# Kernel tuning notes

Measured on AMD Instinct MI355X. Metric: run time of the kernel, lower is better.

Reference implementation:

```python
import math
import jax, jax.numpy as jnp
import numpy as np
from jax import lax

MUL_IN, MUL_OUT = 8, 16
DIM_IN, DIM_OUT = 4 * MUL_IN, 4 * MUL_OUT  # 0e(1) + 1o(3) per multiplicity
DIAMETER = 3.0
STEPS = (1.0, 1.0, 1.0)
NUM_RB = 4
BATCH, GRID = 8, 32


def _lattice():
    r = DIAMETER / 2
    axes = [np.arange(-math.floor(r / s), math.floor(r / s) + 1.0) * s for s in STEPS]
    return jnp.asarray(np.stack(np.meshgrid(*axes, indexing='ij'), axis=-1), jnp.float32)  # [X,Y,Z,3]


def _sus(x):
    # smooth unit step: exp(-1/x) for x>0 else 0
    return jnp.where(x > 0.0, jnp.exp(-1.0 / jnp.where(x > 0.0, x, 1.0)), 0.0)


def _radial_emb(lattice):
    # soft_one_hot_linspace, basis='smooth_finite', cutoff=True
    dist = jnp.linalg.norm(lattice, axis=-1)
    values = jnp.linspace(0.0, DIAMETER / 2, NUM_RB + 2)
    step = values[1] - values[0]
    diff = (dist[..., None] - values[1:-1]) / step
    return 1.14136 * jnp.exp(2.0) * _sus(diff + 1.0) * _sus(1.0 - diff)  # [X,Y,Z,NUM_RB]


def _sph(lattice):
    # real spherical harmonics l=0,1; normalize=True, 'component' normalization
    norm = jnp.linalg.norm(lattice, axis=-1, keepdims=True)
    unit = lattice / jnp.where(norm == 0.0, 1.0, norm)
    sh0 = jnp.ones(lattice.shape[:-1] + (1,), lattice.dtype)
    sh1 = jnp.sqrt(jnp.float32(3.0)) * unit
    return sh0, sh1


def setup_inputs() -> dict:
    key = jax.random.key(0)
    ks = jax.random.split(key, 7)
    x = jax.random.normal(ks[0], (BATCH, GRID, GRID, GRID, DIM_IN), jnp.float32)
    w_lin0 = jax.random.normal(ks[1], (MUL_IN, MUL_OUT), jnp.float32)
    w_lin1 = jax.random.normal(ks[2], (MUL_IN, MUL_OUT), jnp.float32)
    pshape = (NUM_RB, MUL_IN, 1, MUL_OUT)
    w000 = jax.random.normal(ks[3], pshape, jnp.float32)
    w011 = jax.random.normal(ks[4], pshape, jnp.float32)
    w101 = jax.random.normal(ks[5], pshape, jnp.float32)
    w110 = jax.random.normal(ks[6], pshape, jnp.float32)
    return dict(x=x, w_lin0=w_lin0, w_lin1=w_lin1, w000=w000, w011=w011, w101=w101, w110=w110)


def _forward(x, w_lin0, w_lin1, w000, w011, w101, w110):
    lattice = _lattice()
    emb = _radial_emb(lattice)
    sh0, sh1 = _sph(lattice)
    n_lat = lattice.shape[0] * lattice.shape[1] * lattice.shape[2]

    # ---- self-connection: FunctionalLinear(irreps_in -> irreps_out), per-l blocks ----
    lin_norm = 1.0 / math.sqrt(MUL_IN)
    x0 = x[..., :MUL_IN]                                             # [B,X,Y,Z,8]
    x1 = x[..., MUL_IN:].reshape(x.shape[:-1] + (MUL_IN, 3))         # [B,X,Y,Z,8,3]
    sc0 = jnp.einsum('...u,uw->...w', x0, w_lin0) * lin_norm
    sc1 = (jnp.einsum('...ui,uw->...wi', x1, w_lin1) * lin_norm).reshape(x.shape[:-1] + (3 * MUL_OUT,))
    sc = jnp.concatenate([sc0, sc1], axis=-1)                        # [B,X,Y,Z,DIM_OUT]

    # ---- radial weights per lattice point: einsum('xyzk,k...->xyz...') / n_lat ----
    def rad(w):
        return jnp.einsum('xyzk,kuvw->xyzuw', emb, w) / n_lat        # sh mul v == 1 squeezed
    r000, r011, r101, r110 = rad(w000), rad(w011), rad(w101), rad(w110)

    # ---- CG tensor-product 'right': build kernel [X,Y,Z, DIM_IN, DIM_OUT] ----
    inv_s3 = 1.0 / math.sqrt(3.0)  # w3j(0,1,1)=w3j(1,0,1)=w3j(1,1,0)=eye/sqrt(3); w3j(0,0,0)=1
    alpha = 1.0 / math.sqrt(2.0 * MUL_IN)  # 2 paths feed each output irrep, fan mul_in each

    eye3 = jnp.eye(3, dtype=x.dtype)
    # in 0e x sh 0e -> out 0e
    k00 = alpha * r000 * sh0[..., 0][..., None, None]                 # [X,Y,Z,8,16]
    # in 0e x sh 1o -> out 1o
    k01 = (alpha * inv_s3) * jnp.einsum('xyzuw,xyzm->xyzuwm', r011, sh1)
    k01 = k01.reshape(k01.shape[:3] + (MUL_IN, 3 * MUL_OUT))          # [X,Y,Z,8,48]
    # in 1o x sh 1o -> out 0e
    k10 = (alpha * inv_s3) * jnp.einsum('xyzuw,xyzi->xyzuiw', r110, sh1)
    k10 = k10.reshape(k10.shape[:3] + (3 * MUL_IN, MUL_OUT))          # [X,Y,Z,24,16]
    # in 1o x sh 0e -> out 1o
    k11 = (alpha * inv_s3) * jnp.einsum('xyzuw,im->xyzuiwm', r101 * sh0[..., 0][..., None, None], eye3)
    k11 = k11.reshape(k11.shape[:3] + (3 * MUL_IN, 3 * MUL_OUT))      # [X,Y,Z,24,48]

    k = jnp.concatenate([
        jnp.concatenate([k00, k01], axis=-1),
        jnp.concatenate([k10, k11], axis=-1),
    ], axis=-2)                                                       # [X,Y,Z,DIM_IN,DIM_OUT]

    conv = lax.conv_general_dilated(
        lhs=x, rhs=k, window_strides=(1, 1, 1), padding='SAME',
        dimension_numbers=('NXYZC', 'XYZIO', 'NXYZC'))
    return sc + conv


def reference(x, w_lin0, w_lin1, w000, w011, w101, w110):
    return _forward(x, w_lin0, w_lin1, w000, w011, w101, w110)
```

## Files before the change

### kernel.cpp

```cpp
#include <hip/hip_runtime.h>


typedef __attribute__((ext_vector_type(8))) short bf16x8;
typedef __attribute__((ext_vector_type(4))) float f32x4;
typedef unsigned int u32;

__device__ __forceinline__ float sus_f(float v) { return v > 0.f ? __expf(-1.f / v) : 0.f; }

__device__ __forceinline__ unsigned short f2bf(float f) {
    union { float f; unsigned u; } c; c.f = f;
    unsigned u = c.u;
    u += 0x7FFFu + ((u >> 16) & 1u);
    return (unsigned short)(u >> 16);
}

__global__ __launch_bounds__(256) void prep_k(
    const float* __restrict__ w_lin0, const float* __restrict__ w_lin1,
    const float* __restrict__ w000,  const float* __restrict__ w011,
    const float* __restrict__ w101,  const float* __restrict__ w110,
    unsigned short* __restrict__ kw)
{
    const int taps[19] = {1,3,4,5,7,9,10,11,12,13,14,15,16,17,19,21,22,23,25};
    const int ta = blockIdx.x;
    const int t = taps[ta];
    const int a = t / 9, b = (t / 3) % 3, c = t % 3;

    const float fx = (float)(a - 1), fy = (float)(b - 1), fz = (float)(c - 1);
    const float dist = sqrtf(fx * fx + fy * fy + fz * fz);
    float emb[4];
    #pragma unroll
    for (int r = 0; r < 4; ++r) {
        const float v = 0.3f * (float)(r + 1);
        const float d = (dist - v) * (1.0f / 0.3f);
        emb[r] = 8.4335731f * sus_f(d + 1.f) * sus_f(1.f - d);
    }
    const float s = (dist > 0.f) ? (1.7320508f / dist) : 0.f;
    const float shv[3] = { fx * s, fy * s, fz * s };
    const float S000 = 0.25f / 27.f;
    const float S1   = 0.25f * 0.57735027f / 27.f;
    const float LNRM = 0.35355339f;

    const int tid = threadIdx.x;
    const int ci = tid >> 3;

    #pragma unroll
    for (int j = 0; j < 8; ++j) {
        const int o = (tid & 7) * 8 + j;
        float val;
        if (ci < 8) {
            const int u = ci;
            if (o < 16) {
                const float* p = w000 + u * 16 + o;
                val = S000 * (emb[0]*p[0] + emb[1]*p[128] + emb[2]*p[256] + emb[3]*p[384]);
                if (t == 13) val += LNRM * w_lin0[u * 16 + o];
            } else {
                const int oo = o - 16, w = oo / 3, m = oo % 3;
                const float* p = w011 + u * 16 + w;
                val = S1 * shv[m] * (emb[0]*p[0] + emb[1]*p[128] + emb[2]*p[256] + emb[3]*p[384]);
            }
        } else {
            const int iu = ci - 8, u = iu / 3, ic = iu % 3;
            if (o < 16) {
                const float* p = w110 + u * 16 + o;
                val = S1 * shv[ic] * (emb[0]*p[0] + emb[1]*p[128] + emb[2]*p[256] + emb[3]*p[384]);
            } else {
                const int oo = o - 16, w = oo / 3, m = oo % 3;
                if (ic == m) {
                    const float* p = w101 + u * 16 + w;
                    val = S1 * (emb[0]*p[0] + emb[1]*p[128] + emb[2]*p[256] + emb[3]*p[384]);
                    if (t == 13) val += LNRM * w_lin1[u * 16 + w];
                } else {
                    val = 0.f;
                }
            }
        }
        const int g = ci >> 3, slot = ci & 7, nt = o >> 4, cc = o & 15;
        const int lane = (g << 4) | cc;
        kw[((size_t)(ta * 4 + nt) * 64 + lane) * 8 + slot] = f2bf(val);
    }
}

__global__ __launch_bounds__(256) void xcvt(
    const float* __restrict__ x, unsigned short* __restrict__ xb)
{
    const int gi = blockIdx.x * 256 + threadIdx.x;
    const int vox = gi >> 2, g = gi & 3;
    const int gz = vox & 31;
    const float4* sp = reinterpret_cast<const float4*>(x) + (size_t)gi * 2;
    const float4 lo = sp[0], hi = sp[1];
    bf16x8 w;
    w[0] = (short)f2bf(lo.x); w[1] = (short)f2bf(lo.y);
    w[2] = (short)f2bf(lo.z); w[3] = (short)f2bf(lo.w);
    w[4] = (short)f2bf(hi.x); w[5] = (short)f2bf(hi.y);
    w[6] = (short)f2bf(hi.z); w[7] = (short)f2bf(hi.w);
    const int slot = g ^ (((gz + 1) >> 1) & 3);
    const size_t dst = ((size_t)(vox >> 5) << 10) + (gz << 5) + (slot << 3);
    *reinterpret_cast<bf16x8*>(xb + dst) = w;
}

template<bool DIRECT>
__global__ __launch_bounds__(256, 2) void conv_mfma(
    const float* __restrict__ x,
    const unsigned short* __restrict__ xb,
    const unsigned short* __restrict__ kw,
    float* __restrict__ out)
{
    __shared__ unsigned short lx[3 * 10 * 34 * 32];

    const int tid = threadIdx.x;
    const int bid = blockIdx.x;
    const int xcd = bid & 7, idx = bid >> 3;
    const int gid = xcd * 128 + idx;
    const int n = gid >> 7, X = (gid >> 2) & 31, Yg = gid & 3;
    const int Y0 = Yg * 8;
    const int wid = tid >> 6, l = tid & 63, lr = l & 15, lg = l >> 4;

    f32x4* lz = reinterpret_cast<f32x4*>(lx);
    #pragma unroll
    for (int i = 0; i < 16; ++i) {
        const int j = tid + i * 256;
        if (j < 4080) lz[j] = (f32x4)0.f;
    }
    __syncthreads();

    if (DIRECT) {
        #pragma unroll
        for (int k = 0; k < 8; ++k) {
            const int rr = wid + (k << 2);
            if (rr < 30) {
                const int dx = rr / 10, y6 = rr - dx * 10;
                const int gx = X + dx - 1, gy = Y0 + y6 - 1;
                if ((unsigned)gx < 32u && (unsigned)gy < 32u) {
                    const char* src = reinterpret_cast<const char*>(xb) +
                        ((size_t)((n * 32 + gx) * 32 + gy) << 11);
                    char* dstrow = reinterpret_cast<char*>(lx) + rr * 2176 + 64;
                    __builtin_amdgcn_global_load_lds(
                        (const __attribute__((address_space(1))) u32*)(src + l * 16),
                        (__attribute__((address_space(3))) u32*)(dstrow), 16, 0, 0);
                    __builtin_amdgcn_global_load_lds(
                        (const __attribute__((address_space(1))) u32*)(src + 1024 + l * 16),
                        (__attribute__((address_space(3))) u32*)(dstrow + 1024), 16, 0, 0);
                }
            }
        }
    } else {
        for (int it = tid; it < 960; it += 256) {
            const int dx = it / 320, rem = it - dx * 320;
            const int y6 = rem >> 5, z = rem & 31;
            const int gx = X + dx - 1, gy = Y0 + y6 - 1;
            if ((unsigned)gx < 32u && (unsigned)gy < 32u) {
                const float4* sp = reinterpret_cast<const float4*>(
                    x + ((size_t)(((n * 32 + gx) * 32 + gy) * 32 + z) << 5));
                const int swz = ((z + 1) >> 1) & 3;
                char* row = reinterpret_cast<char*>(lx) + (dx * 10 + y6) * 2176 + (z + 1) * 64;
                #pragma unroll
                for (int g = 0; g < 4; ++g) {
                    const float4 lo = sp[2 * g], hi = sp[2 * g + 1];
                    bf16x8 w;
                    w[0] = (short)f2bf(lo.x); w[1] = (short)f2bf(lo.y);
                    w[2] = (short)f2bf(lo.z); w[3] = (short)f2bf(lo.w);
                    w[4] = (short)f2bf(hi.x); w[5] = (short)f2bf(hi.y);
                    w[6] = (short)f2bf(hi.z); w[7] = (short)f2bf(hi.w);
                    *reinterpret_cast<bf16x8*>(row + ((g ^ swz) << 4)) = w;
                }
            }
        }
    }
    __syncthreads();

    constexpr int TA[19] = {1,3,4,5,7,9,10,11,12,13,14,15,16,17,19,21,22,23,25};
    const bf16x8* kwf = reinterpret_cast<const bf16x8*>(kw);
    const char* lxc = reinterpret_cast<const char*>(lx);
    const int yloc = wid * 2;

    f32x4 acc[4][4];
    #pragma unroll
    for (int r = 0; r < 4; ++r)
        #pragma unroll
        for (int nt = 0; nt < 4; ++nt) acc[r][nt] = (f32x4)0.f;

    bf16x8 bcur[4];
    #pragma unroll
    for (int nt = 0; nt < 4; ++nt) bcur[nt] = kwf[(size_t)nt * 64 + l];

    #pragma unroll
    for (int ta = 0; ta < 19; ++ta) {
        const int t = TA[ta];
        const int a = t / 9, b = (t / 3) % 3, c = t % 3;

        bf16x8 bnext[4];
        if (ta < 18) {
            #pragma unroll
            for (int nt = 0; nt < 4; ++nt)
                bnext[nt] = kwf[(size_t)((ta + 1) * 4 + nt) * 64 + l];
        }

        #pragma unroll
        for (int r = 0; r < 4; ++r) {
            const int y10 = yloc + (r >> 1) + b;
            const int zp = 16 * (r & 1) + lr + c;
            const int byte = ((a * 10 + y10) * 34 + zp) * 64 + ((lg ^ ((zp >> 1) & 3)) << 4);
            const bf16x8 af = *reinterpret_cast<const bf16x8*>(lxc + byte);
            #pragma unroll
            for (int nt = 0; nt < 4; ++nt)
                acc[r][nt] = __builtin_amdgcn_mfma_f32_16x16x32_bf16(af, bcur[nt], acc[r][nt], 0, 0, 0);
        }

        if (ta < 18) {
            #pragma unroll
            for (int nt = 0; nt < 4; ++nt) bcur[nt] = bnext[nt];
        }
    }

    float* ob = out + ((size_t)(((n * 32 + X) * 32 + Y0 + yloc) * 32) << 6);
    #pragma unroll
    for (int r = 0; r < 4; ++r) {
        float* oy = ob + (size_t)(r >> 1) * 2048;
        #pragma unroll
        for (int nt = 0; nt < 4; ++nt)
            #pragma unroll
            for (int reg = 0; reg < 4; ++reg) {
                const int z = 16 * (r & 1) + 4 * lg + reg;
                oy[z * 64 + nt * 16 + lr] = acc[r][nt][reg];
            }
    }
}

extern "C" void kernel_launch(void* const* d_in, const int* in_sizes, int n_in,
                              void* d_out, int out_size, void* d_ws, size_t ws_size,
                              hipStream_t stream) {
    const float* x    = (const float*)d_in[0];
    const float* wl0  = (const float*)d_in[1];
    const float* wl1  = (const float*)d_in[2];
    const float* w000 = (const float*)d_in[3];
    const float* w011 = (const float*)d_in[4];
    const float* w101 = (const float*)d_in[5];
    const float* w110 = (const float*)d_in[6];
    float* out = (float*)d_out;

    unsigned short* kw = (unsigned short*)d_ws;
    const size_t KWB = 77824;
    const size_t XBB = 16777216ull;

    prep_k<<<dim3(19), dim3(256), 0, stream>>>(wl0, wl1, w000, w011, w101, w110, kw);

    if (ws_size >= KWB + XBB) {
        unsigned short* xb = (unsigned short*)((char*)d_ws + KWB);
        xcvt<<<dim3(4096), dim3(256), 0, stream>>>(x, xb);
        conv_mfma<true><<<dim3(1024), dim3(256), 0, stream>>>(x, xb, kw, out);
    } else {
        conv_mfma<false><<<dim3(1024), dim3(256), 0, stream>>>(x, nullptr, kw, out);
    }
}
```

Baseline: 45.34 us.

## Merge prep kernels, zero only LDS halos, deepen weight prefetch ring

The weight-prep and input-conversion kernels become one launch, which removes a kernel launch and the gap between them. In the conv kernel, the full LDS zero-fill and its barrier are dropped: only the z-padding columns and out-of-range rows are zeroed, alongside the data loads. B-fragment prefetch changes from one tap ahead to a 4-slot ring kept three taps ahead, and the A-fragment loads are grouped before the MFMAs. The cost is more VGPRs for the ring, which could hurt occupancy at two blocks per SM.

```diff
diff --git a/kernel.cpp b/kernel.cpp
--- a/kernel.cpp
+++ b/kernel.cpp
@@ -14,14 +14,36 @@
     return (unsigned short)(u >> 16);
 }
 
-__global__ __launch_bounds__(256) void prep_k(
+__global__ __launch_bounds__(256) void prep_all(
+    const float* __restrict__ x,
     const float* __restrict__ w_lin0, const float* __restrict__ w_lin1,
     const float* __restrict__ w000,  const float* __restrict__ w011,
     const float* __restrict__ w101,  const float* __restrict__ w110,
-    unsigned short* __restrict__ kw)
+    unsigned short* __restrict__ xb, unsigned short* __restrict__ kw,
+    int koff)
 {
+    const int bid = blockIdx.x;
+    const int tid = threadIdx.x;
+
+    if (bid < koff) {
+        const int gi = bid * 256 + tid;
+        const int vox = gi >> 2, g = gi & 3;
+        const int gz = vox & 31;
+        const float4* sp = reinterpret_cast<const float4*>(x) + (size_t)gi * 2;
+        const float4 lo = sp[0], hi = sp[1];
+        bf16x8 w;
+        w[0] = (short)f2bf(lo.x); w[1] = (short)f2bf(lo.y);
+        w[2] = (short)f2bf(lo.z); w[3] = (short)f2bf(lo.w);
+        w[4] = (short)f2bf(hi.x); w[5] = (short)f2bf(hi.y);
+        w[6] = (short)f2bf(hi.z); w[7] = (short)f2bf(hi.w);
+        const int slot = g ^ (((gz + 1) >> 1) & 3);
+        const size_t dst = ((size_t)(vox >> 5) << 10) + (gz << 5) + (slot << 3);
+        *reinterpret_cast<bf16x8*>(xb + dst) = w;
+        return;
+    }
+
     const int taps[19] = {1,3,4,5,7,9,10,11,12,13,14,15,16,17,19,21,22,23,25};
-    const int ta = blockIdx.x;
+    const int ta = bid - koff;
     const int t = taps[ta];
     const int a = t / 9, b = (t / 3) % 3, c = t % 3;
 
@@ -40,9 +62,7 @@
     const float S1   = 0.25f * 0.57735027f / 27.f;
     const float LNRM = 0.35355339f;
 
-    const int tid = threadIdx.x;
     const int ci = tid >> 3;
-
     #pragma unroll
     for (int j = 0; j < 8; ++j) {
         const int o = (tid & 7) * 8 + j;
@@ -80,24 +100,6 @@
     }
 }
 
-__global__ __launch_bounds__(256) void xcvt(
-    const float* __restrict__ x, unsigned short* __restrict__ xb)
-{
-    const int gi = blockIdx.x * 256 + threadIdx.x;
-    const int vox = gi >> 2, g = gi & 3;
-    const int gz = vox & 31;
-    const float4* sp = reinterpret_cast<const float4*>(x) + (size_t)gi * 2;
-    const float4 lo = sp[0], hi = sp[1];
-    bf16x8 w;
-    w[0] = (short)f2bf(lo.x); w[1] = (short)f2bf(lo.y);
-    w[2] = (short)f2bf(lo.z); w[3] = (short)f2bf(lo.w);
-    w[4] = (short)f2bf(hi.x); w[5] = (short)f2bf(hi.y);
-    w[6] = (short)f2bf(hi.z); w[7] = (short)f2bf(hi.w);
-    const int slot = g ^ (((gz + 1) >> 1) & 3);
-    const size_t dst = ((size_t)(vox >> 5) << 10) + (gz << 5) + (slot << 3);
-    *reinterpret_cast<bf16x8*>(xb + dst) = w;
-}
-
 template<bool DIRECT>
 __global__ __launch_bounds__(256, 2) void conv_mfma(
     const float* __restrict__ x,
@@ -115,13 +117,22 @@
     const int Y0 = Yg * 8;
     const int wid = tid >> 6, l = tid & 63, lr = l & 15, lg = l >> 4;
 
-    f32x4* lz = reinterpret_cast<f32x4*>(lx);
-    #pragma unroll
-    for (int i = 0; i < 16; ++i) {
-        const int j = tid + i * 256;
-        if (j < 4080) lz[j] = (f32x4)0.f;
-    }
-    __syncthreads();
+    const bf16x8* kwf = reinterpret_cast<const bf16x8*>(kw);
+
+    bf16x8 bring[4][4];
+    #pragma unroll
+    for (int p = 0; p < 3; ++p)
+        #pragma unroll
+        for (int nt = 0; nt < 4; ++nt)
+            bring[p][nt] = kwf[(size_t)(p * 4 + nt) * 64 + l];
+
+    if (tid < 60) {
+        const int row = tid >> 1, zp = (tid & 1) * 33;
+        f32x4* dp = reinterpret_cast<f32x4*>(
+            reinterpret_cast<char*>(lx) + row * 2176 + zp * 64);
+        #pragma unroll
+        for (int q = 0; q < 4; ++q) dp[q] = (f32x4)0.f;
+    }
 
     if (DIRECT) {
         #pragma unroll
@@ -130,16 +141,20 @@
             if (rr < 30) {
                 const int dx = rr / 10, y6 = rr - dx * 10;
                 const int gx = X + dx - 1, gy = Y0 + y6 - 1;
+                char* dstrow = reinterpret_cast<char*>(lx) + rr * 2176 + 64;
                 if ((unsigned)gx < 32u && (unsigned)gy < 32u) {
                     const char* src = reinterpret_cast<const char*>(xb) +
                         ((size_t)((n * 32 + gx) * 32 + gy) << 11);
-                    char* dstrow = reinterpret_cast<char*>(lx) + rr * 2176 + 64;
                     __builtin_amdgcn_global_load_lds(
                         (const __attribute__((address_space(1))) u32*)(src + l * 16),
                         (__attribute__((address_space(3))) u32*)(dstrow), 16, 0, 0);
                     __builtin_amdgcn_global_load_lds(
                         (const __attribute__((address_space(1))) u32*)(src + 1024 + l * 16),
                         (__attribute__((address_space(3))) u32*)(dstrow + 1024), 16, 0, 0);
+                } else {
+                    bf16x8 zz = (bf16x8)(short)0;
+                    *reinterpret_cast<bf16x8*>(dstrow + l * 16) = zz;
+                    *reinterpret_cast<bf16x8*>(dstrow + 1024 + l * 16) = zz;
                 }
             }
         }
@@ -148,11 +163,11 @@
             const int dx = it / 320, rem = it - dx * 320;
             const int y6 = rem >> 5, z = rem & 31;
             const int gx = X + dx - 1, gy = Y0 + y6 - 1;
+            char* row = reinterpret_cast<char*>(lx) + (dx * 10 + y6) * 2176 + (z + 1) * 64;
             if ((unsigned)gx < 32u && (unsigned)gy < 32u) {
                 const float4* sp = reinterpret_cast<const float4*>(
                     x + ((size_t)(((n * 32 + gx) * 32 + gy) * 32 + z) << 5));
                 const int swz = ((z + 1) >> 1) & 3;
-                char* row = reinterpret_cast<char*>(lx) + (dx * 10 + y6) * 2176 + (z + 1) * 64;
                 #pragma unroll
                 for (int g = 0; g < 4; ++g) {
                     const float4 lo = sp[2 * g], hi = sp[2 * g + 1];
@@ -163,13 +178,17 @@
                     w[6] = (short)f2bf(hi.z); w[7] = (short)f2bf(hi.w);
                     *reinterpret_cast<bf16x8*>(row + ((g ^ swz) << 4)) = w;
                 }
+            } else {
+                bf16x8 zz = (bf16x8)(short)0;
+                #pragma unroll
+                for (int g = 0; g < 4; ++g)
+                    *reinterpret_cast<bf16x8*>(row + (g << 4)) = zz;
             }
         }
     }
     __syncthreads();
 
     constexpr int TA[19] = {1,3,4,5,7,9,10,11,12,13,14,15,16,17,19,21,22,23,25};
-    const bf16x8* kwf = reinterpret_cast<const bf16x8*>(kw);
     const char* lxc = reinterpret_cast<const char*>(lx);
     const int yloc = wid * 2;
 
@@ -178,38 +197,33 @@
     for (int r = 0; r < 4; ++r)
         #pragma unroll
         for (int nt = 0; nt < 4; ++nt) acc[r][nt] = (f32x4)0.f;
-
-    bf16x8 bcur[4];
-    #pragma unroll
-    for (int nt = 0; nt < 4; ++nt) bcur[nt] = kwf[(size_t)nt * 64 + l];
 
     #pragma unroll
     for (int ta = 0; ta < 19; ++ta) {
         const int t = TA[ta];
         const int a = t / 9, b = (t / 3) % 3, c = t % 3;
 
-        bf16x8 bnext[4];
-        if (ta < 18) {
+        if (ta + 3 < 19) {
             #pragma unroll
             for (int nt = 0; nt < 4; ++nt)
-                bnext[nt] = kwf[(size_t)((ta + 1) * 4 + nt) * 64 + l];
-        }
-
+                bring[(ta + 3) & 3][nt] = kwf[(size_t)((ta + 3) * 4 + nt) * 64 + l];
+        }
+
+        bf16x8 af[4];
         #pragma unroll
         for (int r = 0; r < 4; ++r) {
             const int y10 = yloc + (r >> 1) + b;
             const int zp = 16 * (r & 1) + lr + c;
             const int byte = ((a * 10 + y10) * 34 + zp) * 64 + ((lg ^ ((zp >> 1) & 3)) << 4);
-            const bf16x8 af = *reinterpret_cast<const bf16x8*>(lxc + byte);
+            af[r] = *reinterpret_cast<const bf16x8*>(lxc + byte);
+        }
+
+        #pragma unroll
+        for (int r = 0; r < 4; ++r)
             #pragma unroll
             for (int nt = 0; nt < 4; ++nt)
-                acc[r][nt] = __builtin_amdgcn_mfma_f32_16x16x32_bf16(af, bcur[nt], acc[r][nt], 0, 0, 0);
-        }
-
-        if (ta < 18) {
-            #pragma unroll
-            for (int nt = 0; nt < 4; ++nt) bcur[nt] = bnext[nt];
-        }
+                acc[r][nt] = __builtin_amdgcn_mfma_f32_16x16x32_bf16(
+                    af[r], bring[ta & 3][nt], acc[r][nt], 0, 0, 0);
     }
 
     float* ob = out + ((size_t)(((n * 32 + X) * 32 + Y0 + yloc) * 32) << 6);
@@ -242,13 +256,14 @@
     const size_t KWB = 77824;
     const size_t XBB = 16777216ull;
 
-    prep_k<<<dim3(19), dim3(256), 0, stream>>>(wl0, wl1, w000, w011, w101, w110, kw);
-
     if (ws_size >= KWB + XBB) {
         unsigned short* xb = (unsigned short*)((char*)d_ws + KWB);
-        xcvt<<<dim3(4096), dim3(256), 0, stream>>>(x, xb);
+        prep_all<<<dim3(4096 + 19), dim3(256), 0, stream>>>(
+            x, wl0, wl1, w000, w011, w101, w110, xb, kw, 4096);
         conv_mfma<true><<<dim3(1024), dim3(256), 0, stream>>>(x, xb, kw, out);
     } else {
+        prep_all<<<dim3(19), dim3(256), 0, stream>>>(
+            x, wl0, wl1, w000, w011, w101, w110, nullptr, kw, 0);
         conv_mfma<false><<<dim3(1024), dim3(256), 0, stream>>>(x, nullptr, kw, out);
     }
 }
```

Measured after the change: 42.51 us, median of 2. -6.3%, faster.
